# Optimization experiments

Hardware: AMD Instinct MI355X
Metric: run time of the kernel (lower is better)

## Reference

```python
import jax, jax.numpy as jnp
import numpy as np
import math

DENOM = 32.0

# e3nn scalar_activation normalizes the activation to unit second moment under N(0,1).
# Compute the gelu normalization constant by Gauss-Hermite quadrature.
_zs, _ws = np.polynomial.hermite_e.hermegauss(64)
_g = 0.5 * _zs * (1.0 + np.array([math.erf(z / math.sqrt(2.0)) for z in _zs]))
C_GELU = float(1.0 / math.sqrt((_ws * _g * _g).sum() / math.sqrt(2.0 * math.pi)))


def _spherical_harmonics(r):
    # r: [E,3] unit vectors. Component-normalized real SH for l=1,2,3.
    x, y, z = r[..., 0], r[..., 1], r[..., 2]
    s3, s5, s15 = math.sqrt(3.0), math.sqrt(5.0), math.sqrt(15.0)
    s7, s105 = math.sqrt(7.0), math.sqrt(105.0)
    s35_8, s21_8 = math.sqrt(35.0 / 8.0), math.sqrt(21.0 / 8.0)
    Y1 = s3 * r                                                     # [E,3]
    Y2 = jnp.stack([s15 * x * y, s15 * y * z, 0.5 * s5 * (3 * z * z - 1),
                    s15 * x * z, 0.5 * s15 * (x * x - y * y)], -1)   # [E,5]
    Y3 = jnp.stack([s35_8 * y * (3 * x * x - y * y), s105 * x * y * z,
                    s21_8 * y * (5 * z * z - 1), 0.5 * s7 * z * (5 * z * z - 3),
                    s21_8 * x * (5 * z * z - 1), 0.5 * s105 * z * (x * x - y * y),
                    s35_8 * x * (x * x - 3 * y * y)], -1)            # [E,7]
    return [Y1, Y2, Y3]


def setup_inputs() -> dict:
    key = jax.random.key(0)
    k = jax.random.split(key, 7)
    N, E, MUL, TMUL = 32768, 1048576, 16, 32
    return {
        "x": jax.random.normal(k[0], (N, MUL), jnp.float32),
        "positions": jax.random.normal(k[1], (N, 3), jnp.float32),
        "W_pre": jax.random.normal(k[2], (4, MUL, TMUL), jnp.float32),
        "W_post": jax.random.normal(k[3], (4, TMUL, TMUL), jnp.float32),
        "W_shortcut": jax.random.normal(k[4], (MUL, TMUL), jnp.float32),
        "senders": jax.random.randint(k[5], (E,), 0, N, jnp.int32),
        "receivers": jax.random.randint(k[6], (E,), 0, N, jnp.int32),
    }


def reference(x, positions, W_pre, W_post, W_shortcut, senders, receivers):
    N, mul = x.shape
    tmul = W_pre.shape[-1]
    # --- edge update: sh of relative positions, tensor product with sender scalars ---
    rvec = positions[receivers] - positions[senders]                 # [E,3]
    n = jnp.linalg.norm(rvec, axis=-1, keepdims=True)
    rhat = rvec / jnp.where(n == 0, 1.0, n)
    Ys = _spherical_harmonics(rhat)
    s = x[senders]                                                   # [E,mul] (0e)
    # --- aggregate edge features at receivers (segment sum) ---
    agg = [jax.ops.segment_sum(s, receivers, num_segments=N)]        # 0e block
    for Y in Ys:
        e = (s[:, :, None] * Y[:, None, :]).reshape(s.shape[0], -1)  # 0e x l -> l
        agg.append(jax.ops.segment_sum(e, receivers, num_segments=N).reshape(N, mul, Y.shape[-1]))
    # --- node update: linear_pre -> scalar act -> linear_post, plus shortcut ---
    inv_in = 1.0 / math.sqrt(mul)
    inv_mid = 1.0 / math.sqrt(tmul)
    out = []
    for l in range(4):
        a = agg[l] / DENOM
        if l == 0:
            p = (a @ W_pre[0]) * inv_in
            p = C_GELU * jax.nn.gelu(p, approximate=False)           # act on 0e scalars only
            q = (p @ W_post[0]) * inv_mid
            q = q + (x @ W_shortcut) * inv_in                        # shortcut: only 0e path exists
            out.append(q)
        else:
            p = jnp.einsum('nui,uv->nvi', a, W_pre[l]) * inv_in
            q = jnp.einsum('nvi,vw->nwi', p, W_post[l]) * inv_mid
            out.append(q.reshape(N, -1))
    return jnp.concatenate(out, axis=-1)                              # [N, tmul*16]
```

## Files before the change

kernel.cpp:

```cpp
#include <hip/hip_runtime.h>
#include <math.h>

#define NN 32768
#define EN 1048576
#define NBIN 256
#define BINCAP 8192
#define TILE 4096

#define C_GELU_F 1.5335262f

__global__ __launch_bounds__(512) void bin_k(const int* __restrict__ snd,
                                             const int* __restrict__ rcv,
                                             int* __restrict__ bin_cur,
                                             unsigned* __restrict__ binbuf) {
    __shared__ unsigned cnt[NBIN];
    __shared__ unsigned excl[NBIN];
    __shared__ unsigned cur2[NBIN];
    __shared__ unsigned gbase[NBIN];
    __shared__ unsigned stage[TILE];
    int t = threadIdx.x;
    int tile = blockIdx.x * TILE;
    if (t < NBIN) { cnt[t] = 0; cur2[t] = 0; }
    __syncthreads();

    unsigned w[TILE / 512];
#pragma unroll
    for (int i = 0; i < TILE / 512; ++i) {
        int e = tile + i * 512 + t;
        unsigned r = (unsigned)rcv[e], s = (unsigned)snd[e];
        w[i] = (r << 15) | s;
        atomicAdd(&cnt[w[i] >> 22], 1u);
    }
    __syncthreads();

    unsigned my = (t < NBIN) ? cnt[t] : 0u;
    if (t < NBIN) excl[t] = my;
    __syncthreads();
    for (int d = 1; d < NBIN; d <<= 1) {
        unsigned v = (t < NBIN && t >= d) ? excl[t - d] : 0u;
        __syncthreads();
        if (t < NBIN) excl[t] += v;
        __syncthreads();
    }
    if (t < NBIN) {
        unsigned myexcl = excl[t] - my;
        gbase[t] = atomicAdd((unsigned*)&bin_cur[t], my);
        excl[t] = myexcl;
    }
    __syncthreads();

#pragma unroll
    for (int i = 0; i < TILE / 512; ++i) {
        unsigned b = w[i] >> 22;
        unsigned p = excl[b] + atomicAdd(&cur2[b], 1u);
        stage[p] = w[i];
    }
    __syncthreads();

    for (int p = t; p < TILE; p += 512) {
        unsigned ww = stage[p];
        unsigned b = ww >> 22;
        unsigned idx = gbase[b] + ((unsigned)p - excl[b]);
        if (idx < BINCAP) binbuf[b * BINCAP + idx] = ww;
    }
}

__global__ __launch_bounds__(256) void scan_k(const int* __restrict__ bin_cur,
                                              int* __restrict__ bin_start) {
    __shared__ unsigned sc[NBIN];
    int t = threadIdx.x;
    unsigned my = (unsigned)bin_cur[t];
    sc[t] = my;
    __syncthreads();
    for (int d = 1; d < NBIN; d <<= 1) {
        unsigned v = (t >= d) ? sc[t - d] : 0u;
        __syncthreads();
        sc[t] += v;
        __syncthreads();
    }
    bin_start[t] = (int)(sc[t] - my);
}

__global__ __launch_bounds__(1024) void csr_k(const int* __restrict__ bin_cur,
                                              const int* __restrict__ bin_start,
                                              const unsigned* __restrict__ binbuf,
                                              int* __restrict__ row_ptr,
                                              int* __restrict__ edge_csr) {
    __shared__ unsigned cnt[128];
    __shared__ unsigned excl[128];
    __shared__ unsigned cur2[128];
    int b = blockIdx.x;
    int t = threadIdx.x;
    int M = bin_cur[b]; M = M > BINCAP ? BINCAP : M;
    int base = bin_start[b];
    if (t < 128) { cnt[t] = 0; cur2[t] = 0; }
    __syncthreads();

    const unsigned* bb = binbuf + b * BINCAP;
    for (int i = t; i < M; i += 1024)
        atomicAdd(&cnt[(bb[i] >> 15) & 127], 1u);
    __syncthreads();

    if (t < 128) excl[t] = cnt[t];
    __syncthreads();
    for (int d = 1; d < 128; d <<= 1) {
        unsigned v = (t >= d && t < 128) ? excl[t - d] : 0u;
        __syncthreads();
        if (t < 128) excl[t] += v;
        __syncthreads();
    }
    if (t < 128) {
        unsigned e = excl[t] - cnt[t];
        excl[t] = e;
        row_ptr[(b << 7) + t] = base + (int)e;
        if (b == NBIN - 1 && t == 127) row_ptr[NN] = base + (int)(e + cnt[127]);
    }
    __syncthreads();

    for (int i = t; i < M; i += 1024) {
        unsigned ww = bb[i];
        unsigned r7 = (ww >> 15) & 127;
        unsigned dst = excl[r7] + atomicAdd(&cur2[r7], 1u);
        edge_csr[base + dst] = (int)(ww & 0x7FFF);
    }
}

__global__ __launch_bounds__(256) void pos_k(const float* __restrict__ pos,
                                             float4* __restrict__ posw) {
    int n = blockIdx.x * 256 + threadIdx.x;
    posw[n] = make_float4(pos[3*n], pos[3*n+1], pos[3*n+2], 0.f);
}

#define GROUPS 32
#define BLK 512
#define YST 20
#define GST (16*YST + 8)

__global__ __launch_bounds__(512, 4) void fused_k(const float* __restrict__ x,
                                                  const float4* __restrict__ posw,
                                                  const int* __restrict__ row_ptr,
                                                  const int* __restrict__ edge_csr,
                                                  const float* __restrict__ Wpre,
                                                  const float* __restrict__ Wpost,
                                                  const float* __restrict__ Wsc,
                                                  float* __restrict__ out) {
    __shared__ float sPre[4*516];
    __shared__ float sPost[4*1028];
    __shared__ float sSc[512];
    __shared__ float sY[GROUPS * GST];

    int t = threadIdx.x;
    for (int idx = t; idx < 2048; idx += BLK)
        sPre[(idx >> 9)*516 + (idx & 511)] = Wpre[idx];
    for (int idx = t; idx < 4096; idx += BLK)
        sPost[(idx >> 10)*1028 + (idx & 1023)] = Wpost[idx];
    sSc[t] = Wsc[t];

    int g = t >> 4;
    int j = t & 15;
    int n = blockIdx.x * GROUPS + g;
    int beg = row_ptr[n], end = row_ptr[n + 1];
    int cnt = end - beg;
    float4 rp = posw[n];
    float* yg = sY + g * GST;

    const float s3   = 1.7320508075688772f;
    const float s5   = 2.2360679774997896f;
    const float s15  = 3.8729833462074170f;
    const float s7   = 2.6457513110645907f;
    const float s105 = 10.246950765959598f;
    const float s35_8 = 2.0916500663351889f;
    const float s21_8 = 1.6201851746019651f;

    float acc[16];
#pragma unroll
    for (int u = 0; u < 16; ++u) acc[u] = 0.f;

    int nch = (cnt + 15) >> 4;
    for (int c = 0; c < nch; ++c) {
        int rem = cnt - (c << 4); rem = rem > 16 ? 16 : rem;

        int k = (c << 4) + j;
        int ki = k < cnt ? k : cnt - 1;
        int sE = edge_csr[beg + ki];
        float4 sp = posw[sE];
        float vx = rp.x - sp.x, vy = rp.y - sp.y, vz = rp.z - sp.z;
        float n2 = vx*vx + vy*vy + vz*vz;
        float inv;
        if (n2 > 0.f) {
            inv = rsqrtf(n2);
            inv = inv * (1.5f - 0.5f * n2 * inv * inv);
        } else inv = 0.f;
        float X = vx*inv, Y = vy*inv, Z = vz*inv;
        float XX = X*X, YY = Y*Y, ZZ = Z*Z;

        float* yr = yg + j * YST;
        ((float4*)yr)[0] = make_float4(1.f, s3*X, s3*Y, s3*Z);
        ((float4*)yr)[1] = make_float4(s15*X*Y, s15*Y*Z,
                                       0.5f*s5*(3.f*ZZ - 1.f), s15*X*Z);
        ((float4*)yr)[2] = make_float4(0.5f*s15*(XX - YY),
                                       s35_8*Y*(3.f*XX - YY),
                                       s105*X*Y*Z,
                                       s21_8*Y*(5.f*ZZ - 1.f));
        ((float4*)yr)[3] = make_float4(0.5f*s7*Z*(5.f*ZZ - 3.f),
                                       s21_8*X*(5.f*ZZ - 1.f),
                                       0.5f*s105*Z*(XX - YY),
                                       s35_8*X*(XX - 3.f*YY));

#pragma unroll 4
        for (int e = 0; e < rem; ++e) {
            int se = __shfl(sE, (t & 48) + e, 64);
            float y = yg[e * YST + j];
            const float4* xp = (const float4*)(x + (se << 4));
            float4 a0 = xp[0], a1 = xp[1], a2 = xp[2], a3 = xp[3];
            acc[0]  += a0.x * y;  acc[1]  += a0.y * y;
            acc[2]  += a0.z * y;  acc[3]  += a0.w * y;
            acc[4]  += a1.x * y;  acc[5]  += a1.y * y;
            acc[6]  += a1.z * y;  acc[7]  += a1.w * y;
            acc[8]  += a2.x * y;  acc[9]  += a2.y * y;
            acc[10] += a2.z * y;  acc[11] += a2.w * y;
            acc[12] += a3.x * y;  acc[13] += a3.y * y;
            acc[14] += a3.z * y;  acc[15] += a3.w * y;
        }
    }
    __syncthreads();

    int l, i, offl, deg;
    if (j == 0)      { l = 0; i = 0;     offl = 0;   deg = 1; }
    else if (j < 4)  { l = 1; i = j - 1; offl = 32;  deg = 3; }
    else if (j < 9)  { l = 2; i = j - 4; offl = 128; deg = 5; }
    else             { l = 3; i = j - 9; offl = 288; deg = 7; }

    const float c1 = 0.0078125f;
    const float c2 = 0.17677669529663687f;

    float p[32];
#pragma unroll
    for (int v = 0; v < 32; ++v) p[v] = 0.f;
    const float* wp = sPre + l * 516;
#pragma unroll
    for (int uu = 0; uu < 16; ++uu) {
        float a = acc[uu];
        const float4* w4 = (const float4*)(wp + (uu << 5));
#pragma unroll
        for (int vq = 0; vq < 8; ++vq) {
            float4 w = w4[vq];
            p[4*vq+0] += a * w.x;
            p[4*vq+1] += a * w.y;
            p[4*vq+2] += a * w.z;
            p[4*vq+3] += a * w.w;
        }
    }
#pragma unroll
    for (int v = 0; v < 32; ++v) p[v] *= c1;

    if (j == 0) {
#pragma unroll
        for (int v = 0; v < 32; ++v) {
            float pv = p[v];
            p[v] = C_GELU_F * 0.5f * pv * (1.f + erff(pv * 0.7071067811865476f));
        }
    }

    float q[32];
#pragma unroll
    for (int w = 0; w < 32; ++w) q[w] = 0.f;
    const float* wq = sPost + l * 1028;
#pragma unroll
    for (int v = 0; v < 32; ++v) {
        float pv = p[v];
        const float4* w4 = (const float4*)(wq + (v << 5));
#pragma unroll
        for (int wd = 0; wd < 8; ++wd) {
            float4 w = w4[wd];
            q[4*wd+0] += pv * w.x;
            q[4*wd+1] += pv * w.y;
            q[4*wd+2] += pv * w.z;
            q[4*wd+3] += pv * w.w;
        }
    }
#pragma unroll
    for (int w = 0; w < 32; ++w) q[w] *= c2;

    if (j == 0) {
        const float* xp = x + (n << 4);
#pragma unroll
        for (int uu = 0; uu < 16; ++uu) {
            float xv = 0.25f * xp[uu];
            const float4* w4 = (const float4*)(sSc + (uu << 5));
#pragma unroll
            for (int wd = 0; wd < 8; ++wd) {
                float4 w = w4[wd];
                q[4*wd+0] += xv * w.x;
                q[4*wd+1] += xv * w.y;
                q[4*wd+2] += xv * w.z;
                q[4*wd+3] += xv * w.w;
            }
        }
    }

    float* op = out + (n << 9) + offl + i;
#pragma unroll
    for (int w = 0; w < 32; ++w) op[w * deg] = q[w];
}

extern "C" void kernel_launch(void* const* d_in, const int* in_sizes, int n_in,
                              void* d_out, int out_size, void* d_ws, size_t ws_size,
                              hipStream_t stream) {
    const float* x     = (const float*)d_in[0];
    const float* pos   = (const float*)d_in[1];
    const float* Wpre  = (const float*)d_in[2];
    const float* Wpost = (const float*)d_in[3];
    const float* Wsc   = (const float*)d_in[4];
    const int*   snd   = (const int*)d_in[5];
    const int*   rcv   = (const int*)d_in[6];
    float* out = (float*)d_out;

    char* ws = (char*)d_ws;
    int*      bin_cur   = (int*)(ws);
    int*      bin_start = (int*)(ws + 1024);
    int*      row_ptr   = (int*)(ws + 2048);
    float4*   posw      = (float4*)(ws + 0x30000);
    int*      edge_csr  = (int*)(ws + 0xB0000);
    unsigned* binbuf    = (unsigned*)(ws + 0x500000);

    hipMemsetAsync(bin_cur, 0, NBIN * sizeof(int), stream);
    bin_k<<<EN / TILE, 512, 0, stream>>>(snd, rcv, bin_cur, binbuf);
    scan_k<<<1, 256, 0, stream>>>(bin_cur, bin_start);
    csr_k<<<NBIN, 1024, 0, stream>>>(bin_cur, bin_start, binbuf, row_ptr, edge_csr);
    pos_k<<<NN / 256, 256, 0, stream>>>(pos, posw);
    fused_k<<<NN / GROUPS, BLK, 0, stream>>>(x, posw, row_ptr, edge_csr,
                                             Wpre, Wpost, Wsc, out);
}
```

Measured before the change: 199.6 us.

## Merge small kernels and software-pipeline edge gather in fused kernel

New measurement: 186.1 us. 1.07x faster.

```diff
diff --git a/kernel.cpp b/kernel.cpp
--- a/kernel.cpp
+++ b/kernel.cpp
@@ -11,6 +11,8 @@
 
 __global__ __launch_bounds__(512) void bin_k(const int* __restrict__ snd,
                                              const int* __restrict__ rcv,
+                                             const float* __restrict__ pos,
+                                             float4* __restrict__ posw,
                                              int* __restrict__ bin_cur,
                                              unsigned* __restrict__ binbuf) {
     __shared__ unsigned cnt[NBIN];
@@ -21,6 +23,10 @@
     int t = threadIdx.x;
     int tile = blockIdx.x * TILE;
     if (t < NBIN) { cnt[t] = 0; cur2[t] = 0; }
+    if (t < 128) {
+        int n = (blockIdx.x << 7) + t;
+        posw[n] = make_float4(pos[3*n], pos[3*n+1], pos[3*n+2], 0.f);
+    }
     __syncthreads();
 
     unsigned w[TILE / 512];
@@ -65,34 +71,28 @@
     }
 }
 
-__global__ __launch_bounds__(256) void scan_k(const int* __restrict__ bin_cur,
-                                              int* __restrict__ bin_start) {
-    __shared__ unsigned sc[NBIN];
-    int t = threadIdx.x;
-    unsigned my = (unsigned)bin_cur[t];
-    sc[t] = my;
-    __syncthreads();
-    for (int d = 1; d < NBIN; d <<= 1) {
-        unsigned v = (t >= d) ? sc[t - d] : 0u;
-        __syncthreads();
-        sc[t] += v;
-        __syncthreads();
-    }
-    bin_start[t] = (int)(sc[t] - my);
-}
-
 __global__ __launch_bounds__(1024) void csr_k(const int* __restrict__ bin_cur,
-                                              const int* __restrict__ bin_start,
                                               const unsigned* __restrict__ binbuf,
                                               int* __restrict__ row_ptr,
                                               int* __restrict__ edge_csr) {
+    __shared__ unsigned sc[NBIN];
     __shared__ unsigned cnt[128];
     __shared__ unsigned excl[128];
     __shared__ unsigned cur2[128];
     int b = blockIdx.x;
     int t = threadIdx.x;
-    int M = bin_cur[b]; M = M > BINCAP ? BINCAP : M;
-    int base = bin_start[b];
+
+    if (t < NBIN) sc[t] = (unsigned)bin_cur[t];
+    __syncthreads();
+    for (int d = 1; d < NBIN; d <<= 1) {
+        unsigned v = (t < NBIN && t >= d) ? sc[t - d] : 0u;
+        __syncthreads();
+        if (t < NBIN) sc[t] += v;
+        __syncthreads();
+    }
+    int Mraw = bin_cur[b];
+    int base = (int)(sc[b] - (unsigned)Mraw);
+    int M = Mraw > BINCAP ? BINCAP : Mraw;
     if (t < 128) { cnt[t] = 0; cur2[t] = 0; }
     __syncthreads();
 
@@ -123,12 +123,6 @@
         unsigned dst = excl[r7] + atomicAdd(&cur2[r7], 1u);
         edge_csr[base + dst] = (int)(ww & 0x7FFF);
     }
-}
-
-__global__ __launch_bounds__(256) void pos_k(const float* __restrict__ pos,
-                                             float4* __restrict__ posw) {
-    int n = blockIdx.x * 256 + threadIdx.x;
-    posw[n] = make_float4(pos[3*n], pos[3*n+1], pos[3*n+2], 0.f);
 }
 
 #define GROUPS 32
@@ -155,6 +149,7 @@
     for (int idx = t; idx < 4096; idx += BLK)
         sPost[(idx >> 10)*1028 + (idx & 1023)] = Wpost[idx];
     sSc[t] = Wsc[t];
+    __syncthreads();
 
     int g = t >> 4;
     int j = t & 15;
@@ -177,53 +172,69 @@
     for (int u = 0; u < 16; ++u) acc[u] = 0.f;
 
     int nch = (cnt + 15) >> 4;
-    for (int c = 0; c < nch; ++c) {
-        int rem = cnt - (c << 4); rem = rem > 16 ? 16 : rem;
-
-        int k = (c << 4) + j;
-        int ki = k < cnt ? k : cnt - 1;
-        int sE = edge_csr[beg + ki];
+    if (nch > 0) {
+        int ki0 = (j < cnt) ? j : cnt - 1;
+        int sE = edge_csr[beg + ki0];
         float4 sp = posw[sE];
-        float vx = rp.x - sp.x, vy = rp.y - sp.y, vz = rp.z - sp.z;
-        float n2 = vx*vx + vy*vy + vz*vz;
-        float inv;
-        if (n2 > 0.f) {
-            inv = rsqrtf(n2);
-            inv = inv * (1.5f - 0.5f * n2 * inv * inv);
-        } else inv = 0.f;
-        float X = vx*inv, Y = vy*inv, Z = vz*inv;
-        float XX = X*X, YY = Y*Y, ZZ = Z*Z;
-
-        float* yr = yg + j * YST;
-        ((float4*)yr)[0] = make_float4(1.f, s3*X, s3*Y, s3*Z);
-        ((float4*)yr)[1] = make_float4(s15*X*Y, s15*Y*Z,
-                                       0.5f*s5*(3.f*ZZ - 1.f), s15*X*Z);
-        ((float4*)yr)[2] = make_float4(0.5f*s15*(XX - YY),
-                                       s35_8*Y*(3.f*XX - YY),
-                                       s105*X*Y*Z,
-                                       s21_8*Y*(5.f*ZZ - 1.f));
-        ((float4*)yr)[3] = make_float4(0.5f*s7*Z*(5.f*ZZ - 3.f),
-                                       s21_8*X*(5.f*ZZ - 1.f),
-                                       0.5f*s105*Z*(XX - YY),
-                                       s35_8*X*(XX - 3.f*YY));
-
-#pragma unroll 4
-        for (int e = 0; e < rem; ++e) {
-            int se = __shfl(sE, (t & 48) + e, 64);
-            float y = yg[e * YST + j];
-            const float4* xp = (const float4*)(x + (se << 4));
-            float4 a0 = xp[0], a1 = xp[1], a2 = xp[2], a3 = xp[3];
-            acc[0]  += a0.x * y;  acc[1]  += a0.y * y;
-            acc[2]  += a0.z * y;  acc[3]  += a0.w * y;
-            acc[4]  += a1.x * y;  acc[5]  += a1.y * y;
-            acc[6]  += a1.z * y;  acc[7]  += a1.w * y;
-            acc[8]  += a2.x * y;  acc[9]  += a2.y * y;
-            acc[10] += a2.z * y;  acc[11] += a2.w * y;
-            acc[12] += a3.x * y;  acc[13] += a3.y * y;
-            acc[14] += a3.z * y;  acc[15] += a3.w * y;
-        }
-    }
-    __syncthreads();
+
+        for (int c = 0; c < nch; ++c) {
+            int kn = ((c + 1) << 4) + j;
+            int kiN = (kn < cnt) ? kn : cnt - 1;
+            int sEn = edge_csr[beg + kiN];
+
+            float vx = rp.x - sp.x, vy = rp.y - sp.y, vz = rp.z - sp.z;
+            float n2 = vx*vx + vy*vy + vz*vz;
+            float inv;
+            if (n2 > 0.f) {
+                inv = rsqrtf(n2);
+                inv = inv * (1.5f - 0.5f * n2 * inv * inv);
+            } else inv = 0.f;
+            float X = vx*inv, Y = vy*inv, Z = vz*inv;
+            float XX = X*X, YY = Y*Y, ZZ = Z*Z;
+            float m = (((c << 4) + j) < cnt) ? 1.f : 0.f;
+
+            float* yr = yg + j * YST;
+            ((float4*)yr)[0] = make_float4(m, m*(s3*X), m*(s3*Y), m*(s3*Z));
+            ((float4*)yr)[1] = make_float4(m*(s15*X*Y), m*(s15*Y*Z),
+                                           m*(0.5f*s5*(3.f*ZZ - 1.f)), m*(s15*X*Z));
+            ((float4*)yr)[2] = make_float4(m*(0.5f*s15*(XX - YY)),
+                                           m*(s35_8*Y*(3.f*XX - YY)),
+                                           m*(s105*X*Y*Z),
+                                           m*(s21_8*Y*(5.f*ZZ - 1.f)));
+            ((float4*)yr)[3] = make_float4(m*(0.5f*s7*Z*(5.f*ZZ - 3.f)),
+                                           m*(s21_8*X*(5.f*ZZ - 1.f)),
+                                           m*(0.5f*s105*Z*(XX - YY)),
+                                           m*(s35_8*X*(XX - 3.f*YY)));
+
+            int se[16];
+#pragma unroll
+            for (int e = 0; e < 16; ++e)
+                se[e] = __shfl(sE, (t & 48) + e, 64);
+            float yt[16];
+#pragma unroll
+            for (int e = 0; e < 16; ++e)
+                yt[e] = yg[e * YST + j];
+
+            float4 spn = posw[sEn];
+
+#pragma unroll
+            for (int e = 0; e < 16; ++e) {
+                float y = yt[e];
+                const float4* xp = (const float4*)(x + (se[e] << 4));
+                float4 a0 = xp[0], a1 = xp[1], a2 = xp[2], a3 = xp[3];
+                acc[0]  += a0.x * y;  acc[1]  += a0.y * y;
+                acc[2]  += a0.z * y;  acc[3]  += a0.w * y;
+                acc[4]  += a1.x * y;  acc[5]  += a1.y * y;
+                acc[6]  += a1.z * y;  acc[7]  += a1.w * y;
+                acc[8]  += a2.x * y;  acc[9]  += a2.y * y;
+                acc[10] += a2.z * y;  acc[11] += a2.w * y;
+                acc[12] += a3.x * y;  acc[13] += a3.y * y;
+                acc[14] += a3.z * y;  acc[15] += a3.w * y;
+            }
+
+            sE = sEn; sp = spn;
+        }
+    }
 
     int l, i, offl, deg;
     if (j == 0)      { l = 0; i = 0;     offl = 0;   deg = 1; }
@@ -318,17 +329,14 @@
 
     char* ws = (char*)d_ws;
     int*      bin_cur   = (int*)(ws);
-    int*      bin_start = (int*)(ws + 1024);
     int*      row_ptr   = (int*)(ws + 2048);
     float4*   posw      = (float4*)(ws + 0x30000);
     int*      edge_csr  = (int*)(ws + 0xB0000);
     unsigned* binbuf    = (unsigned*)(ws + 0x500000);
 
     hipMemsetAsync(bin_cur, 0, NBIN * sizeof(int), stream);
-    bin_k<<<EN / TILE, 512, 0, stream>>>(snd, rcv, bin_cur, binbuf);
-    scan_k<<<1, 256, 0, stream>>>(bin_cur, bin_start);
-    csr_k<<<NBIN, 1024, 0, stream>>>(bin_cur, bin_start, binbuf, row_ptr, edge_csr);
-    pos_k<<<NN / 256, 256, 0, stream>>>(pos, posw);
+    bin_k<<<EN / TILE, 512, 0, stream>>>(snd, rcv, pos, posw, bin_cur, binbuf);
+    csr_k<<<NBIN, 1024, 0, stream>>>(bin_cur, binbuf, row_ptr, edge_csr);
     fused_k<<<NN / GROUPS, BLK, 0, stream>>>(x, posw, row_ptr, edge_csr,
                                              Wpre, Wpost, Wsc, out);
 }
```
